# Kernel tuning notes

Hardware: AMD Instinct MI355X
Metric: run time of the kernel (lower is better)

The kernel has to match this reference:

```python
import jax, jax.numpy as jnp
import numpy as np

N_ITER = 4  # n_iter
NEG = -1e9  # masked-score fill (softmax-safe stand-in for -inf)


def _mfvi(x, mask, ternary, global_):
    """MFVI message passing between head (H) and node (Z) variables with global nodes.

    x:       [B, L, D] unary scores for Z nodes
    mask:    [B, L]    padding mask (nonzero = valid token)
    ternary: [D, D, H] ternary factor scores f(Z_i=a, Z_j=b, H-channel c)
    global_: [G, D, H] global-node factor scores
    Defaults: norm=softmax, regularize=1, stepsize=1, damping=0, async_update,
    no tensor decomposition, mode='all-attn', block_msg=False, output_prob=False.
    """
    B, L, D = x.shape
    m1 = (mask != 0)                                             # [B, L]
    pair_valid = m1[:, None, :, None] & m1[:, None, None, :]     # [B, 1, L, L]
    unary = x                                                    # pos_embed='none'
    Qz = jax.nn.softmax(unary, axis=-1)                          # [B, L, D]
    F_Z = unary
    neg = jnp.asarray(NEG, x.dtype)
    for _ in range(N_ITER):
        # --- H update: scores for head variable H_{i,c} over candidate heads j ---
        # F_Hs[n,h,i,j] = sum_{a,b} Qz[n,i,a] * ternary[a,b,h] * Qz[n,j,b]
        F_Hs = jnp.einsum('nia,abh,njb->nhij', Qz, ternary, Qz)  # [B, H, L, L]
        F_Hs = jnp.where(pair_valid, F_Hs, neg)
        # global-node columns: F_Hg[n,h,i,g] = sum_a Qz[n,i,a] * global_[g,a,h]
        F_Hg = jnp.einsum('nia,gah->nhig', Qz, global_)          # [B, H, L, G]
        F_H = jnp.concatenate([F_Hs, F_Hg], axis=-1)             # [B, H, L, L+G]
        Q_H = jax.nn.softmax(F_H, axis=-1)                       # regularize_H = 1
        Qhs, Qhg = Q_H[..., :L], Q_H[..., L:]
        # --- Z update (async: uses fresh Q_H) ---
        # message to Z_i from its chosen head j
        msg_i = jnp.einsum('nhij,njb,abh->nia', Qhs, Qz, ternary)
        # message to Z_j from dependents i (block_msg=False keeps it)
        msg_j = jnp.einsum('nhij,nia,abh->njb', Qhs, Qz, ternary)
        # message to Z_i from global nodes
        msg_g = jnp.einsum('nhig,gah->nia', Qhg, global_)
        F_Z = unary + msg_i + msg_j + msg_g                      # [B, L, D]
        Qz = jax.nn.softmax(F_Z, axis=-1)                        # regularize_Z = 1
    # output_prob=False -> unnormalized scores, zeroed at padding
    return jnp.where(m1[..., None], F_Z, jnp.zeros_like(F_Z))


def setup_inputs() -> dict:
    key = jax.random.key(0)
    k1, k2, k3 = jax.random.split(key, 3)
    B, L, D, H, G = 4, 1024, 128, 8, 64
    x = jax.random.normal(k1, (B, L, D), dtype=jnp.float32)
    mask = jnp.ones((B, L), dtype=jnp.int32)
    ternary = jax.random.normal(k2, (D, D, H), dtype=jnp.float32)          # init std=1
    global_ = jax.random.normal(k3, (G, D, H), dtype=jnp.float32) / np.sqrt(D)
    return {"x": x, "mask": mask, "ternary": ternary, "global_": global_}


def reference(x, mask, ternary, global_):
    return _mfvi(x, mask, ternary, global_)
```

## Files before the change

### kernel.cpp

```cpp
#include <hip/hip_runtime.h>
#include <math.h>

#define Bn 4
#define Ln 1024
#define Dn 128
#define Hn 8
#define Gn 64
#define NITERS 4

typedef _Float16 f16;
typedef _Float16 half8 __attribute__((ext_vector_type(8)));
typedef _Float16 half4v __attribute__((ext_vector_type(4)));
typedef float floatx4 __attribute__((ext_vector_type(4)));

#define WPAD 136
#define PPAD 72

#define MFMA(a, b, c) __builtin_amdgcn_mfma_f32_16x16x32_f16((a), (b), (c), 0, 0, 0)

__device__ __forceinline__ void gl_lds16(const f16* g, f16* l) {
    __builtin_amdgcn_global_load_lds(
        (const __attribute__((address_space(1))) void*)(g),
        (__attribute__((address_space(3))) void*)(l),
        16, 0, 0);
}

__device__ __forceinline__ void issue_tiles(const f16* us, const f16* ub, int sb,
                                            f16* UsB, f16* UbB, int w, int l) {
    #pragma unroll
    for (int k = 0; k < 4; k++) {
        int c = w * 4 + k;
        {
            int r = c * 4 + (l >> 4); int g = (l & 15) ^ (r & 7);
            gl_lds16(us + (size_t)r * Dn + g * 8, UsB + c * 512);
        }
        {
            int r = c * 8 + (l >> 3); int g = (l & 7) ^ (r & 7);
            gl_lds16(ub + (size_t)r * sb + g * 8, UbB + c * 512);
        }
    }
}

__global__ void repack_kernel(const float* __restrict__ ter, const float* __restrict__ glb,
                              f16* __restrict__ TpA, f16* __restrict__ TpB,
                              f16* __restrict__ GpA, f16* __restrict__ Gpt) {
    int idx = blockIdx.x * 256 + threadIdx.x;
    if (idx < Dn * Dn * Hn) {
        int h = idx % Hn; int b = (idx / Hn) % Dn; int a = idx / (Hn * Dn);
        f16 v = (f16)ter[idx];
        TpA[((size_t)h * Dn + a) * Dn + b] = v;
        TpB[((size_t)h * Dn + b) * Dn + a] = v;
    }
    if (idx < Gn * Dn * Hn) {
        int h = idx % Hn; int a = (idx / Hn) % Dn; int g = idx / (Hn * Dn);
        f16 v = (f16)glb[idx];
        GpA[((size_t)h * Gn + g) * Dn + a] = v;
        Gpt[((size_t)h * Dn + a) * Gn + g] = v;
    }
}

__global__ void softmax_rows_kernel(const float* __restrict__ in, f16* __restrict__ out) {
    int row = blockIdx.x;
    int t = threadIdx.x;
    __shared__ float red[2];
    float v = in[(size_t)row * Dn + t];
    float m = v;
    #pragma unroll
    for (int off = 1; off < 64; off <<= 1) m = fmaxf(m, __shfl_xor(m, off, 64));
    if ((t & 63) == 0) red[t >> 6] = m;
    __syncthreads();
    m = fmaxf(red[0], red[1]);
    float e = __expf(v - m);
    float s = e;
    #pragma unroll
    for (int off = 1; off < 64; off <<= 1) s += __shfl_xor(s, off, 64);
    __syncthreads();
    if ((t & 63) == 0) red[t >> 6] = s;
    __syncthreads();
    s = red[0] + red[1];
    out[(size_t)row * Dn + t] = (f16)(e / s);
}

__launch_bounds__(256, 4)
__global__ void uv_kernel(const f16* __restrict__ Qz, const f16* __restrict__ TpA,
                          const f16* __restrict__ TpB,
                          f16* __restrict__ U, f16* __restrict__ Ut, f16* __restrict__ Vt) {
    int bx = blockIdx.x;
    int h  = blockIdx.y;
    int n  = blockIdx.z;
    int t  = threadIdx.x;
    int w = t >> 6, l = t & 63, m = l & 15, q = l >> 4;

    __shared__ __align__(16) f16 Ts[128 * WPAD];

    const f16* qbase = Qz + ((size_t)n * Ln + bx * 64 + w * 16 + m) * Dn;
    half8 aq[4];
    #pragma unroll
    for (int ks = 0; ks < 4; ks++)
        aq[ks] = *(const half8*)(qbase + ks * 32 + q * 8);

    size_t hoff = (size_t)(n * Hn + h);
    int jr0 = bx * 64 + w * 16 + 4 * q;

    {
        const f16* src = TpA + (size_t)h * Dn * Dn;
        for (int ii = 0; ii < 8; ii++) {
            int idx = t + 256 * ii; int r = idx >> 4, c = idx & 15;
            *(float4*)&Ts[r * WPAD + c * 8] = *(const float4*)(src + (size_t)r * Dn + c * 8);
        }
        __syncthreads();
    }
    #pragma unroll
    for (int ct = 0; ct < 8; ct++) {
        floatx4 acc = {0.f, 0.f, 0.f, 0.f};
        #pragma unroll
        for (int ks = 0; ks < 4; ks++) {
            half8 b = *(const half8*)&Ts[(ct * 16 + m) * WPAD + ks * 32 + q * 8];
            acc = MFMA(aq[ks], b, acc);
        }
        half4v pk = { (f16)acc[0], (f16)acc[1], (f16)acc[2], (f16)acc[3] };
        *(half4v*)(Ut + (hoff * Dn + ct * 16 + m) * Ln + jr0) = pk;
    }
    f16* urow = U + (hoff * Ln + (size_t)(bx * 64 + w * 16 + m)) * Dn;
    #pragma unroll
    for (int at = 0; at < 8; at++) {
        floatx4 acc = {0.f, 0.f, 0.f, 0.f};
        #pragma unroll
        for (int ks = 0; ks < 4; ks++) {
            half8 aT = *(const half8*)&Ts[(at * 16 + m) * WPAD + ks * 32 + q * 8];
            acc = MFMA(aT, aq[ks], acc);
        }
        half4v pk = { (f16)acc[0], (f16)acc[1], (f16)acc[2], (f16)acc[3] };
        *(half4v*)(urow + at * 16 + 4 * q) = pk;
    }
    __syncthreads();
    {
        const f16* src = TpB + (size_t)h * Dn * Dn;
        for (int ii = 0; ii < 8; ii++) {
            int idx = t + 256 * ii; int r = idx >> 4, c = idx & 15;
            *(float4*)&Ts[r * WPAD + c * 8] = *(const float4*)(src + (size_t)r * Dn + c * 8);
        }
        __syncthreads();
    }
    #pragma unroll
    for (int ct = 0; ct < 8; ct++) {
        floatx4 acc = {0.f, 0.f, 0.f, 0.f};
        #pragma unroll
        for (int ks = 0; ks < 4; ks++) {
            half8 b = *(const half8*)&Ts[(ct * 16 + m) * WPAD + ks * 32 + q * 8];
            acc = MFMA(aq[ks], b, acc);
        }
        half4v pk = { (f16)acc[0], (f16)acc[1], (f16)acc[2], (f16)acc[3] };
        *(half4v*)(Vt + (hoff * Dn + ct * 16 + m) * Ln + jr0) = pk;
    }
}

__launch_bounds__(256, 2)
__global__ void msgi_kernel(const f16* __restrict__ Qz, const f16* __restrict__ U,
                            const f16* __restrict__ Ut, const f16* __restrict__ GpA,
                            const f16* __restrict__ Gpt, const int* __restrict__ mask,
                            f16* __restrict__ Macc, float* __restrict__ rowLinv) {
    int it = blockIdx.x, h = blockIdx.y, n = blockIdx.z;
    int t = threadIdx.x;
    int w = t >> 6, l = t & 63, m = l & 15, q = l >> 4;
    int rh = w >> 1, ch = w & 1;
    int ih = w >> 1, ah = w & 1;

    __shared__ __align__(16) f16 Us[2][64 * 128];
    __shared__ __align__(16) f16 Ub[2][128 * 64];
    __shared__ __align__(16) f16 Ps[64 * PPAD];
    __shared__ int jms[2][64];
    __shared__ float lpart[2][64];
    __shared__ float linvS[64];

    half8 bq[2][4];
    #pragma unroll
    for (int ib = 0; ib < 2; ib++) {
        const f16* qr = Qz + ((size_t)n * Ln + it * 64 + ch * 32 + ib * 16 + m) * Dn;
        #pragma unroll
        for (int ks = 0; ks < 4; ks++)
            bq[ib][ks] = *(const half8*)(qr + ks * 32 + q * 8);
    }
    int im[2];
    #pragma unroll
    for (int ib = 0; ib < 2; ib++)
        im[ib] = mask[n * Ln + it * 64 + ch * 32 + ib * 16 + m];

    float lacc[2] = {0.f, 0.f};
    floatx4 Oacc[2][4];
    #pragma unroll
    for (int ib = 0; ib < 2; ib++)
        #pragma unroll
        for (int at = 0; at < 4; at++) Oacc[ib][at] = (floatx4){0.f, 0.f, 0.f, 0.f};

    size_t hoff = (size_t)(n * Hn + h);

    issue_tiles(U + hoff * Ln * Dn, Ut + hoff * Dn * Ln, Ln, Us[0], Ub[0], w, l);
    if (t < 64) jms[0][t] = mask[n * Ln + t];
    __syncthreads();

    for (int jt = 0; jt < 17; jt++) {
        int cur = jt & 1, nxt = cur ^ 1;
        if (jt + 1 < 17) {
            const f16 *us, *ub; int sb;
            if (jt + 1 < 16) {
                us = U + (hoff * Ln + (size_t)(jt + 1) * 64) * Dn;
                ub = Ut + hoff * Dn * Ln + (jt + 1) * 64;
                sb = Ln;
            } else {
                us = GpA + (size_t)h * Gn * Dn;
                ub = Gpt + (size_t)h * Dn * Gn;
                sb = Gn;
            }
            issue_tiles(us, ub, sb, Us[nxt], Ub[nxt], w, l);
            if (t < 64) jms[nxt][t] = (jt + 1 < 16) ? mask[n * Ln + (jt + 1) * 64 + t] : 1;
        }
        int isg = (jt == 16);
        #pragma unroll
        for (int jb = 0; jb < 2; jb++) {
            int r0 = rh * 32 + jb * 16 + m;
            half8 au[4];
            #pragma unroll
            for (int ks = 0; ks < 4; ks++)
                au[ks] = *(const half8*)&Us[cur][((size_t)r0 << 7) + ((((ks << 2) + q)) ^ (r0 & 7)) * 8];
            int jmr[4];
            #pragma unroll
            for (int reg = 0; reg < 4; reg++)
                jmr[reg] = jms[cur][rh * 32 + jb * 16 + 4 * q + reg];
            #pragma unroll
            for (int ib = 0; ib < 2; ib++) {
                floatx4 s = {0.f, 0.f, 0.f, 0.f};
                #pragma unroll
                for (int ks = 0; ks < 4; ks++) s = MFMA(au[ks], bq[ib][ks], s);
                half4v pk;
                #pragma unroll
                for (int reg = 0; reg < 4; reg++) {
                    float p = (isg || (im[ib] && jmr[reg])) ? __expf(fminf(s[reg], 11.f)) : 0.f;
                    lacc[ib] += p;
                    pk[reg] = (f16)p;
                }
                *(half4v*)&Ps[(ch * 32 + ib * 16 + m) * PPAD + rh * 32 + jb * 16 + 4 * q] = pk;
            }
        }
        __syncthreads();

        #pragma unroll
        for (int kst = 0; kst < 2; kst++) {
            half8 aP[2];
            #pragma unroll
            for (int ib = 0; ib < 2; ib++)
                aP[ib] = *(const half8*)&Ps[(ih * 32 + ib * 16 + m) * PPAD + kst * 32 + q * 8];
            #pragma unroll
            for (int at = 0; at < 4; at++) {
                int r0 = ah * 64 + at * 16 + m;
                half8 bU = *(const half8*)&Ub[cur][((size_t)r0 << 6) + ((((kst << 2) + q)) ^ (r0 & 7)) * 8];
                #pragma unroll
                for (int ib = 0; ib < 2; ib++)
                    Oacc[ib][at] = MFMA(aP[ib], bU, Oacc[ib][at]);
            }
        }
        __syncthreads();
    }

    #pragma unroll
    for (int ib = 0; ib < 2; ib++) {
        float v = lacc[ib];
        v += __shfl_xor(v, 16, 64);
        v += __shfl_xor(v, 32, 64);
        lacc[ib] = v;
    }
    if (q == 0) {
        lpart[rh][ch * 32 + m] = lacc[0];
        lpart[rh][ch * 32 + 16 + m] = lacc[1];
    }
    __syncthreads();
    size_t rbase = hoff * Ln + (size_t)it * 64;
    if (t < 64) {
        float inv = 1.0f / (lpart[0][t] + lpart[1][t]);
        linvS[t] = inv;
        int mk = mask[n * Ln + it * 64 + t];
        rowLinv[rbase + t] = mk ? inv : 0.f;
    }
    __syncthreads();
    f16* Mo = Macc + rbase * Dn;
    #pragma unroll
    for (int ib = 0; ib < 2; ib++)
        #pragma unroll
        for (int reg = 0; reg < 4; reg++) {
            int row = ih * 32 + ib * 16 + 4 * q + reg;
            float inv = linvS[row];
            #pragma unroll
            for (int at = 0; at < 4; at++)
                Mo[(size_t)row * Dn + ah * 64 + at * 16 + m] = (f16)(Oacc[ib][at][reg] * inv);
        }
}

__launch_bounds__(256, 2)
__global__ void msgj_kernel(const f16* __restrict__ Qz, const f16* __restrict__ U,
                            const f16* __restrict__ Vt, const int* __restrict__ mask,
                            const float* __restrict__ rowLinv, f16* __restrict__ Macc) {
    int jt = blockIdx.x, h = blockIdx.y, n = blockIdx.z;
    int t = threadIdx.x;
    int w = t >> 6, l = t & 63, m = l & 15, q = l >> 4;
    int ihs = w >> 1, jhs = w & 1;
    int jh2 = w >> 1, bh = w & 1;

    __shared__ __align__(16) f16 Qs[2][64 * 128];
    __shared__ __align__(16) f16 Vb[2][128 * 64];
    __shared__ __align__(16) f16 Psj[64 * PPAD];
    __shared__ float lvS[2][64];

    size_t hoff = (size_t)(n * Hn + h);

    half8 bu[2][4];
    #pragma unroll
    for (int jb = 0; jb < 2; jb++) {
        const f16* ur = U + (hoff * Ln + (size_t)jt * 64 + jhs * 32 + jb * 16 + m) * Dn;
        #pragma unroll
        for (int ks = 0; ks < 4; ks++)
            bu[jb][ks] = *(const half8*)(ur + ks * 32 + q * 8);
    }
    int jm[2];
    #pragma unroll
    for (int jb = 0; jb < 2; jb++)
        jm[jb] = mask[n * Ln + jt * 64 + jhs * 32 + jb * 16 + m];

    floatx4 Oacc[2][4];
    #pragma unroll
    for (int jb = 0; jb < 2; jb++)
        #pragma unroll
        for (int bt = 0; bt < 4; bt++) Oacc[jb][bt] = (floatx4){0.f, 0.f, 0.f, 0.f};

    issue_tiles(Qz + (size_t)n * Ln * Dn, Vt + hoff * Dn * Ln, Ln, Qs[0], Vb[0], w, l);
    if (t < 64) lvS[0][t] = rowLinv[hoff * Ln + t];
    __syncthreads();

    for (int it2 = 0; it2 < 16; it2++) {
        int cur = it2 & 1, nxt = cur ^ 1;
        if (it2 + 1 < 16) {
            issue_tiles(Qz + ((size_t)n * Ln + (size_t)(it2 + 1) * 64) * Dn,
                        Vt + hoff * Dn * Ln + (it2 + 1) * 64, Ln, Qs[nxt], Vb[nxt], w, l);
            if (t < 64) lvS[nxt][t] = rowLinv[hoff * Ln + (it2 + 1) * 64 + t];
        }
        #pragma unroll
        for (int ib = 0; ib < 2; ib++) {
            int r0 = ihs * 32 + ib * 16 + m;
            half8 aq2[4];
            #pragma unroll
            for (int ks = 0; ks < 4; ks++)
                aq2[ks] = *(const half8*)&Qs[cur][((size_t)r0 << 7) + ((((ks << 2) + q)) ^ (r0 & 7)) * 8];
            float lv[4];
            #pragma unroll
            for (int reg = 0; reg < 4; reg++)
                lv[reg] = lvS[cur][ihs * 32 + ib * 16 + 4 * q + reg];
            #pragma unroll
            for (int jb = 0; jb < 2; jb++) {
                floatx4 s = {0.f, 0.f, 0.f, 0.f};
                #pragma unroll
                for (int ks = 0; ks < 4; ks++) s = MFMA(aq2[ks], bu[jb][ks], s);
                half4v pk;
                #pragma unroll
                for (int reg = 0; reg < 4; reg++) {
                    float p = jm[jb] ? __expf(fminf(s[reg], 11.f)) * lv[reg] : 0.f;
                    pk[reg] = (f16)p;
                }
                *(half4v*)&Psj[(jhs * 32 + jb * 16 + m) * PPAD + ihs * 32 + ib * 16 + 4 * q] = pk;
            }
        }
        __syncthreads();

        #pragma unroll
        for (int kst = 0; kst < 2; kst++) {
            half8 aP[2];
            #pragma unroll
            for (int jb = 0; jb < 2; jb++)
                aP[jb] = *(const half8*)&Psj[(jh2 * 32 + jb * 16 + m) * PPAD + kst * 32 + q * 8];
            #pragma unroll
            for (int bt = 0; bt < 4; bt++) {
                int r0 = bh * 64 + bt * 16 + m;
                half8 bV = *(const half8*)&Vb[cur][((size_t)r0 << 6) + ((((kst << 2) + q)) ^ (r0 & 7)) * 8];
                #pragma unroll
                for (int jb = 0; jb < 2; jb++)
                    Oacc[jb][bt] = MFMA(aP[jb], bV, Oacc[jb][bt]);
            }
        }
        __syncthreads();
    }

    f16* Mo = Macc + (hoff * Ln + (size_t)jt * 64) * Dn;
    #pragma unroll
    for (int jb = 0; jb < 2; jb++)
        #pragma unroll
        for (int reg = 0; reg < 4; reg++) {
            int row = jh2 * 32 + jb * 16 + 4 * q + reg;
            #pragma unroll
            for (int bt = 0; bt < 4; bt++) {
                f16* p = &Mo[(size_t)row * Dn + bh * 64 + bt * 16 + m];
                *p = (f16)((float)*p + Oacc[jb][bt][reg]);
            }
        }
}

__global__ void combine_kernel(const float* __restrict__ x, const f16* __restrict__ Macc,
                               const int* __restrict__ mask, float* __restrict__ out,
                               f16* __restrict__ Qzh, int do_softmax, int do_mask) {
    int t = threadIdx.x;
    int half = t >> 7;
    int t2 = t & 127;
    int row = blockIdx.x * 2 + half;
    __shared__ float red[4];
    int n = row >> 10;
    float acc = x[(size_t)row * Dn + t2];
    const f16* mp = Macc + (size_t)n * Hn * Ln * Dn + (size_t)(row & 1023) * Dn + t2;
    #pragma unroll
    for (int h = 0; h < Hn; h++) acc += (float)mp[(size_t)h * Ln * Dn];
    float o = acc;
    if (do_mask && mask[row] == 0) o = 0.f;
    out[(size_t)row * Dn + t2] = o;
    if (do_softmax) {
        float m = acc;
        #pragma unroll
        for (int off = 1; off < 64; off <<= 1) m = fmaxf(m, __shfl_xor(m, off, 64));
        if ((t & 63) == 0) red[t >> 6] = m;
        __syncthreads();
        m = fmaxf(red[2 * half], red[2 * half + 1]);
        float e = __expf(acc - m);
        float s = e;
        #pragma unroll
        for (int off = 1; off < 64; off <<= 1) s += __shfl_xor(s, off, 64);
        __syncthreads();
        if ((t & 63) == 0) red[t >> 6] = s;
        __syncthreads();
        s = red[2 * half] + red[2 * half + 1];
        Qzh[(size_t)row * Dn + t2] = (f16)(e / s);
    }
}

extern "C" void kernel_launch(void* const* d_in, const int* in_sizes, int n_in,
                              void* d_out, int out_size, void* d_ws, size_t ws_size,
                              hipStream_t stream) {
    const float* x       = (const float*)d_in[0];
    const int*   mask    = (const int*)d_in[1];
    const float* ternary = (const float*)d_in[2];
    const float* global_ = (const float*)d_in[3];
    float* out = (float*)d_out;
    (void)ws_size; (void)n_in; (void)in_sizes; (void)out_size;

    char* ws = (char*)d_ws;
    size_t o = 0;
    f16* Qzh = (f16*)(ws + o); o += (size_t)Bn * Ln * Dn * 2;
    f16* U   = (f16*)(ws + o); o += (size_t)Bn * Hn * Ln * Dn * 2;
    f16* Ut  = (f16*)(ws + o); o += (size_t)Bn * Hn * Ln * Dn * 2;
    f16* Vt  = (f16*)(ws + o); o += (size_t)Bn * Hn * Ln * Dn * 2;
    f16* TpA = (f16*)(ws + o); o += (size_t)Hn * Dn * Dn * 2;
    f16* TpB = (f16*)(ws + o); o += (size_t)Hn * Dn * Dn * 2;
    f16* GpA = (f16*)(ws + o); o += (size_t)Hn * Gn * Dn * 2;
    f16* Gpt = (f16*)(ws + o); o += (size_t)Hn * Dn * Gn * 2;
    float* rowLinv = (float*)(ws + o); o += (size_t)Bn * Hn * Ln * 4;
    f16* Macc = (f16*)(ws + o); o += (size_t)Bn * Hn * Ln * Dn * 2;

    repack_kernel<<<(Dn * Dn * Hn + 255) / 256, 256, 0, stream>>>(ternary, global_, TpA, TpB, GpA, Gpt);
    softmax_rows_kernel<<<Bn * Ln, 128, 0, stream>>>(x, Qzh);

    for (int it = 0; it < NITERS; it++) {
        uv_kernel<<<dim3(Ln / 64, Hn, Bn), 256, 0, stream>>>(Qzh, TpA, TpB, U, Ut, Vt);
        msgi_kernel<<<dim3(Ln / 64, Hn, Bn), 256, 0, stream>>>(Qzh, U, Ut, GpA, Gpt, mask, Macc, rowLinv);
        msgj_kernel<<<dim3(Ln / 64, Hn, Bn), 256, 0, stream>>>(Qzh, U, Vt, mask, rowLinv, Macc);
        combine_kernel<<<Bn * Ln / 2, 256, 0, stream>>>(x, Macc, mask, out, Qzh,
                                                        (it < NITERS - 1) ? 1 : 0,
                                                        (it == NITERS - 1) ? 1 : 0);
    }
}
```

Measured before the change: 400.6 us.

## Give each warp a private Ub/Vb slice and drop the trailing per-tile barrier

In msgi and msgj, the second GEMM's output is now split by D columns per warp, so each warp reads only its own 32-row slice of the Ub/Vb tile. The warp can then reload that slice itself right after use, so the Ub/Vb buffer drops from double to single buffering. The P buffer becomes double-buffered instead, which lets the second __syncthreads per tile iteration be removed. In exchange, each warp re-reads all 64 P rows, and each warp's private reload is exposed because it is not prefetched a full iteration ahead.

After: 400.7 us. Within noise of the previous version (+0.0%).

```diff
diff --git a/kernel.cpp b/kernel.cpp
--- a/kernel.cpp
+++ b/kernel.cpp
@@ -25,19 +25,21 @@
         16, 0, 0);
 }
 
-__device__ __forceinline__ void issue_tiles(const f16* us, const f16* ub, int sb,
-                                            f16* UsB, f16* UbB, int w, int l) {
+__device__ __forceinline__ void issue_us(const f16* us, f16* UsB, int w, int l) {
     #pragma unroll
     for (int k = 0; k < 4; k++) {
         int c = w * 4 + k;
-        {
-            int r = c * 4 + (l >> 4); int g = (l & 15) ^ (r & 7);
-            gl_lds16(us + (size_t)r * Dn + g * 8, UsB + c * 512);
-        }
-        {
-            int r = c * 8 + (l >> 3); int g = (l & 7) ^ (r & 7);
-            gl_lds16(ub + (size_t)r * sb + g * 8, UbB + c * 512);
-        }
+        int r = c * 4 + (l >> 4); int g = (l & 15) ^ (r & 7);
+        gl_lds16(us + (size_t)r * Dn + g * 8, UsB + c * 512);
+    }
+}
+
+__device__ __forceinline__ void issue_ub_priv(const f16* ub, int sb, f16* UbB, int w, int l) {
+    #pragma unroll
+    for (int k = 0; k < 4; k++) {
+        int r = w * 32 + k * 8 + (l >> 3);
+        int g = (l & 7) ^ (r & 7);
+        gl_lds16(ub + (size_t)r * sb + g * 8, UbB + (w * 32 + k * 8) * 64);
     }
 }
 
@@ -164,11 +166,10 @@
     int t = threadIdx.x;
     int w = t >> 6, l = t & 63, m = l & 15, q = l >> 4;
     int rh = w >> 1, ch = w & 1;
-    int ih = w >> 1, ah = w & 1;
 
     __shared__ __align__(16) f16 Us[2][64 * 128];
-    __shared__ __align__(16) f16 Ub[2][128 * 64];
-    __shared__ __align__(16) f16 Ps[64 * PPAD];
+    __shared__ __align__(16) f16 Ub[128 * 64];
+    __shared__ __align__(16) f16 Ps[2][64 * PPAD];
     __shared__ int jms[2][64];
     __shared__ float lpart[2][64];
     __shared__ float linvS[64];
@@ -187,32 +188,26 @@
         im[ib] = mask[n * Ln + it * 64 + ch * 32 + ib * 16 + m];
 
     float lacc[2] = {0.f, 0.f};
-    floatx4 Oacc[2][4];
-    #pragma unroll
-    for (int ib = 0; ib < 2; ib++)
-        #pragma unroll
-        for (int at = 0; at < 4; at++) Oacc[ib][at] = (floatx4){0.f, 0.f, 0.f, 0.f};
+    floatx4 Oacc[4][2];
+    #pragma unroll
+    for (int ib = 0; ib < 4; ib++) {
+        Oacc[ib][0] = (floatx4){0.f, 0.f, 0.f, 0.f};
+        Oacc[ib][1] = (floatx4){0.f, 0.f, 0.f, 0.f};
+    }
 
     size_t hoff = (size_t)(n * Hn + h);
 
-    issue_tiles(U + hoff * Ln * Dn, Ut + hoff * Dn * Ln, Ln, Us[0], Ub[0], w, l);
+    issue_us(U + hoff * Ln * Dn, Us[0], w, l);
+    issue_ub_priv(Ut + hoff * Dn * Ln, Ln, Ub, w, l);
     if (t < 64) jms[0][t] = mask[n * Ln + t];
     __syncthreads();
 
     for (int jt = 0; jt < 17; jt++) {
-        int cur = jt & 1, nxt = cur ^ 1;
+        int cur = jt & 1, nxt = cur ^ 1, pb = jt & 1;
         if (jt + 1 < 17) {
-            const f16 *us, *ub; int sb;
-            if (jt + 1 < 16) {
-                us = U + (hoff * Ln + (size_t)(jt + 1) * 64) * Dn;
-                ub = Ut + hoff * Dn * Ln + (jt + 1) * 64;
-                sb = Ln;
-            } else {
-                us = GpA + (size_t)h * Gn * Dn;
-                ub = Gpt + (size_t)h * Dn * Gn;
-                sb = Gn;
-            }
-            issue_tiles(us, ub, sb, Us[nxt], Ub[nxt], w, l);
+            const f16* us = (jt + 1 < 16) ? U + (hoff * Ln + (size_t)(jt + 1) * 64) * Dn
+                                          : GpA + (size_t)h * Gn * Dn;
+            issue_us(us, Us[nxt], w, l);
             if (t < 64) jms[nxt][t] = (jt + 1 < 16) ? mask[n * Ln + (jt + 1) * 64 + t] : 1;
         }
         int isg = (jt == 16);
@@ -239,27 +234,33 @@
                     lacc[ib] += p;
                     pk[reg] = (f16)p;
                 }
-                *(half4v*)&Ps[(ch * 32 + ib * 16 + m) * PPAD + rh * 32 + jb * 16 + 4 * q] = pk;
+                *(half4v*)&Ps[pb][(ch * 32 + ib * 16 + m) * PPAD + rh * 32 + jb * 16 + 4 * q] = pk;
             }
         }
         __syncthreads();
 
         #pragma unroll
         for (int kst = 0; kst < 2; kst++) {
-            half8 aP[2];
-            #pragma unroll
-            for (int ib = 0; ib < 2; ib++)
-                aP[ib] = *(const half8*)&Ps[(ih * 32 + ib * 16 + m) * PPAD + kst * 32 + q * 8];
-            #pragma unroll
-            for (int at = 0; at < 4; at++) {
-                int r0 = ah * 64 + at * 16 + m;
-                half8 bU = *(const half8*)&Ub[cur][((size_t)r0 << 6) + ((((kst << 2) + q)) ^ (r0 & 7)) * 8];
-                #pragma unroll
-                for (int ib = 0; ib < 2; ib++)
-                    Oacc[ib][at] = MFMA(aP[ib], bU, Oacc[ib][at]);
+            half8 aP[4];
+            #pragma unroll
+            for (int ib = 0; ib < 4; ib++)
+                aP[ib] = *(const half8*)&Ps[pb][(ib * 16 + m) * PPAD + kst * 32 + q * 8];
+            #pragma unroll
+            for (int bt = 0; bt < 2; bt++) {
+                int r0 = w * 32 + bt * 16 + m;
+                half8 bU = *(const half8*)&Ub[((size_t)r0 << 6) + ((((kst << 2) + q)) ^ (r0 & 7)) * 8];
+                #pragma unroll
+                for (int ib = 0; ib < 4; ib++)
+                    Oacc[ib][bt] = MFMA(aP[ib], bU, Oacc[ib][bt]);
             }
         }
-        __syncthreads();
+        if (jt + 1 < 17) {
+            __builtin_amdgcn_sched_barrier(0);
+            const f16* ub; int sb;
+            if (jt + 1 < 16) { ub = Ut + hoff * Dn * Ln + (jt + 1) * 64; sb = Ln; }
+            else             { ub = Gpt + (size_t)h * Dn * Gn;           sb = Gn; }
+            issue_ub_priv(ub, sb, Ub, w, l);
+        }
     }
 
     #pragma unroll
@@ -284,14 +285,14 @@
     __syncthreads();
     f16* Mo = Macc + rbase * Dn;
     #pragma unroll
-    for (int ib = 0; ib < 2; ib++)
+    for (int ib = 0; ib < 4; ib++)
         #pragma unroll
         for (int reg = 0; reg < 4; reg++) {
-            int row = ih * 32 + ib * 16 + 4 * q + reg;
+            int row = ib * 16 + 4 * q + reg;
             float inv = linvS[row];
             #pragma unroll
-            for (int at = 0; at < 4; at++)
-                Mo[(size_t)row * Dn + ah * 64 + at * 16 + m] = (f16)(Oacc[ib][at][reg] * inv);
+            for (int bt = 0; bt < 2; bt++)
+                Mo[(size_t)row * Dn + w * 32 + bt * 16 + m] = (f16)(Oacc[ib][bt][reg] * inv);
         }
 }
 
@@ -303,11 +304,10 @@
     int t = threadIdx.x;
     int w = t >> 6, l = t & 63, m = l & 15, q = l >> 4;
     int ihs = w >> 1, jhs = w & 1;
-    int jh2 = w >> 1, bh = w & 1;
 
     __shared__ __align__(16) f16 Qs[2][64 * 128];
-    __shared__ __align__(16) f16 Vb[2][128 * 64];
-    __shared__ __align__(16) f16 Psj[64 * PPAD];
+    __shared__ __align__(16) f16 Vb[128 * 64];
+    __shared__ __align__(16) f16 Psj[2][64 * PPAD];
     __shared__ float lvS[2][64];
 
     size_t hoff = (size_t)(n * Hn + h);
@@ -325,21 +325,22 @@
     for (int jb = 0; jb < 2; jb++)
         jm[jb] = mask[n * Ln + jt * 64 + jhs * 32 + jb * 16 + m];
 
-    floatx4 Oacc[2][4];
-    #pragma unroll
-    for (int jb = 0; jb < 2; jb++)
-        #pragma unroll
-        for (int bt = 0; bt < 4; bt++) Oacc[jb][bt] = (floatx4){0.f, 0.f, 0.f, 0.f};
-
-    issue_tiles(Qz + (size_t)n * Ln * Dn, Vt + hoff * Dn * Ln, Ln, Qs[0], Vb[0], w, l);
+    floatx4 Oacc[4][2];
+    #pragma unroll
+    for (int jb = 0; jb < 4; jb++) {
+        Oacc[jb][0] = (floatx4){0.f, 0.f, 0.f, 0.f};
+        Oacc[jb][1] = (floatx4){0.f, 0.f, 0.f, 0.f};
+    }
+
+    issue_us(Qz + (size_t)n * Ln * Dn, Qs[0], w, l);
+    issue_ub_priv(Vt + hoff * Dn * Ln, Ln, Vb, w, l);
     if (t < 64) lvS[0][t] = rowLinv[hoff * Ln + t];
     __syncthreads();
 
     for (int it2 = 0; it2 < 16; it2++) {
-        int cur = it2 & 1, nxt = cur ^ 1;
+        int cur = it2 & 1, nxt = cur ^ 1, pb = it2 & 1;
         if (it2 + 1 < 16) {
-            issue_tiles(Qz + ((size_t)n * Ln + (size_t)(it2 + 1) * 64) * Dn,
-                        Vt + hoff * Dn * Ln + (it2 + 1) * 64, Ln, Qs[nxt], Vb[nxt], w, l);
+            issue_us(Qz + ((size_t)n * Ln + (size_t)(it2 + 1) * 64) * Dn, Qs[nxt], w, l);
             if (t < 64) lvS[nxt][t] = rowLinv[hoff * Ln + (it2 + 1) * 64 + t];
         }
         #pragma unroll
@@ -364,38 +365,41 @@
                     float p = jm[jb] ? __expf(fminf(s[reg], 11.f)) * lv[reg] : 0.f;
                     pk[reg] = (f16)p;
                 }
-                *(half4v*)&Psj[(jhs * 32 + jb * 16 + m) * PPAD + ihs * 32 + ib * 16 + 4 * q] = pk;
+                *(half4v*)&Psj[pb][(jhs * 32 + jb * 16 + m) * PPAD + ihs * 32 + ib * 16 + 4 * q] = pk;
             }
         }
         __syncthreads();
 
         #pragma unroll
         for (int kst = 0; kst < 2; kst++) {
-            half8 aP[2];
-            #pragma unroll
-            for (int jb = 0; jb < 2; jb++)
-                aP[jb] = *(const half8*)&Psj[(jh2 * 32 + jb * 16 + m) * PPAD + kst * 32 + q * 8];
-            #pragma unroll
-            for (int bt = 0; bt < 4; bt++) {
-                int r0 = bh * 64 + bt * 16 + m;
-                half8 bV = *(const half8*)&Vb[cur][((size_t)r0 << 6) + ((((kst << 2) + q)) ^ (r0 & 7)) * 8];
-                #pragma unroll
-                for (int jb = 0; jb < 2; jb++)
+            half8 aP[4];
+            #pragma unroll
+            for (int jb = 0; jb < 4; jb++)
+                aP[jb] = *(const half8*)&Psj[pb][(jb * 16 + m) * PPAD + kst * 32 + q * 8];
+            #pragma unroll
+            for (int bt = 0; bt < 2; bt++) {
+                int r0 = w * 32 + bt * 16 + m;
+                half8 bV = *(const half8*)&Vb[((size_t)r0 << 6) + ((((kst << 2) + q)) ^ (r0 & 7)) * 8];
+                #pragma unroll
+                for (int jb = 0; jb < 4; jb++)
                     Oacc[jb][bt] = MFMA(aP[jb], bV, Oacc[jb][bt]);
             }
         }
-        __syncthreads();
+        if (it2 + 1 < 16) {
+            __builtin_amdgcn_sched_barrier(0);
+            issue_ub_priv(Vt + hoff * Dn * Ln + (it2 + 1) * 64, Ln, Vb, w, l);
+        }
     }
 
     f16* Mo = Macc + (hoff * Ln + (size_t)jt * 64) * Dn;
     #pragma unroll
-    for (int jb = 0; jb < 2; jb++)
+    for (int jb = 0; jb < 4; jb++)
         #pragma unroll
         for (int reg = 0; reg < 4; reg++) {
-            int row = jh2 * 32 + jb * 16 + 4 * q + reg;
-            #pragma unroll
-            for (int bt = 0; bt < 4; bt++) {
-                f16* p = &Mo[(size_t)row * Dn + bh * 64 + bt * 16 + m];
+            int row = jb * 16 + 4 * q + reg;
+            #pragma unroll
+            for (int bt = 0; bt < 2; bt++) {
+                f16* p = &Mo[(size_t)row * Dn + w * 32 + bt * 16 + m];
                 *p = (f16)((float)*p + Oacc[jb][bt][reg]);
             }
         }
```

## Halve query tile in msgi/msgj, drop double buffering, raise occupancy

Applied to the files above, without the earlier changes.

The msgi and msgj kernels now process 32 query rows per block instead of 64, doubling the grid. They drop LDS double-buffering in favour of single buffers loaded synchronously each step, and swizzle the P tile instead of padding it. Launch bounds go from 2 to 4 blocks per CU. The aim is more occupancy and parallelism from less LDS and fewer registers per block, at the cost of losing copy/compute overlap and reloading every key/value tile twice as many times overall.

Measured after the change: 434.9 us. 1.09x slower.

```diff
diff --git a/kernel.cpp b/kernel.cpp
--- a/kernel.cpp
+++ b/kernel.cpp
@@ -14,7 +14,6 @@
 typedef float floatx4 __attribute__((ext_vector_type(4)));
 
 #define WPAD 136
-#define PPAD 72
 
 #define MFMA(a, b, c) __builtin_amdgcn_mfma_f32_16x16x32_f16((a), (b), (c), 0, 0, 0)
 
@@ -25,19 +24,21 @@
         16, 0, 0);
 }
 
-__device__ __forceinline__ void issue_tiles(const f16* us, const f16* ub, int sb,
-                                            f16* UsB, f16* UbB, int w, int l) {
+__device__ __forceinline__ void issue_us(const f16* us, f16* UsB, int w, int l) {
     #pragma unroll
     for (int k = 0; k < 4; k++) {
         int c = w * 4 + k;
-        {
-            int r = c * 4 + (l >> 4); int g = (l & 15) ^ (r & 7);
-            gl_lds16(us + (size_t)r * Dn + g * 8, UsB + c * 512);
-        }
-        {
-            int r = c * 8 + (l >> 3); int g = (l & 7) ^ (r & 7);
-            gl_lds16(ub + (size_t)r * sb + g * 8, UbB + c * 512);
-        }
+        int r = c * 4 + (l >> 4); int g = (l & 15) ^ (r & 7);
+        gl_lds16(us + (size_t)r * Dn + g * 8, UsB + c * 512);
+    }
+}
+
+__device__ __forceinline__ void issue_ub_full(const f16* ub, int sb, f16* UbB, int w, int l) {
+    #pragma unroll
+    for (int k = 0; k < 4; k++) {
+        int c = w * 4 + k;
+        int r = c * 8 + (l >> 3); int g = (l & 7) ^ (r & 7);
+        gl_lds16(ub + (size_t)r * sb + g * 8, UbB + c * 512);
     }
 }
 
@@ -155,7 +156,7 @@
     }
 }
 
-__launch_bounds__(256, 2)
+__launch_bounds__(256, 4)
 __global__ void msgi_kernel(const f16* __restrict__ Qz, const f16* __restrict__ U,
                             const f16* __restrict__ Ut, const f16* __restrict__ GpA,
                             const f16* __restrict__ Gpt, const int* __restrict__ mask,
@@ -166,239 +167,195 @@
     int rh = w >> 1, ch = w & 1;
     int ih = w >> 1, ah = w & 1;
 
-    __shared__ __align__(16) f16 Us[2][64 * 128];
-    __shared__ __align__(16) f16 Ub[2][128 * 64];
-    __shared__ __align__(16) f16 Ps[64 * PPAD];
-    __shared__ int jms[2][64];
-    __shared__ float lpart[2][64];
-    __shared__ float linvS[64];
-
-    half8 bq[2][4];
-    #pragma unroll
-    for (int ib = 0; ib < 2; ib++) {
-        const f16* qr = Qz + ((size_t)n * Ln + it * 64 + ch * 32 + ib * 16 + m) * Dn;
-        #pragma unroll
-        for (int ks = 0; ks < 4; ks++)
-            bq[ib][ks] = *(const half8*)(qr + ks * 32 + q * 8);
-    }
-    int im[2];
-    #pragma unroll
-    for (int ib = 0; ib < 2; ib++)
-        im[ib] = mask[n * Ln + it * 64 + ch * 32 + ib * 16 + m];
-
-    float lacc[2] = {0.f, 0.f};
-    floatx4 Oacc[2][4];
-    #pragma unroll
-    for (int ib = 0; ib < 2; ib++)
-        #pragma unroll
-        for (int at = 0; at < 4; at++) Oacc[ib][at] = (floatx4){0.f, 0.f, 0.f, 0.f};
+    __shared__ __align__(16) f16 Us[64 * 128];
+    __shared__ __align__(16) f16 Ub[128 * 64];
+    __shared__ __align__(16) f16 Ps[32 * 64];
+    __shared__ int jms[64];
+    __shared__ float lpart[2][32];
+    __shared__ float linvS[32];
+
+    const f16* qr = Qz + ((size_t)n * Ln + it * 32 + ch * 16 + m) * Dn;
+    half8 bq[4];
+    #pragma unroll
+    for (int ks = 0; ks < 4; ks++)
+        bq[ks] = *(const half8*)(qr + ks * 32 + q * 8);
+    int im = mask[n * Ln + it * 32 + ch * 16 + m];
+
+    float lacc = 0.f;
+    floatx4 Oacc[4];
+    #pragma unroll
+    for (int at = 0; at < 4; at++) Oacc[at] = (floatx4){0.f, 0.f, 0.f, 0.f};
 
     size_t hoff = (size_t)(n * Hn + h);
 
-    issue_tiles(U + hoff * Ln * Dn, Ut + hoff * Dn * Ln, Ln, Us[0], Ub[0], w, l);
-    if (t < 64) jms[0][t] = mask[n * Ln + t];
-    __syncthreads();
-
     for (int jt = 0; jt < 17; jt++) {
-        int cur = jt & 1, nxt = cur ^ 1;
-        if (jt + 1 < 17) {
-            const f16 *us, *ub; int sb;
-            if (jt + 1 < 16) {
-                us = U + (hoff * Ln + (size_t)(jt + 1) * 64) * Dn;
-                ub = Ut + hoff * Dn * Ln + (jt + 1) * 64;
-                sb = Ln;
-            } else {
-                us = GpA + (size_t)h * Gn * Dn;
-                ub = Gpt + (size_t)h * Dn * Gn;
-                sb = Gn;
-            }
-            issue_tiles(us, ub, sb, Us[nxt], Ub[nxt], w, l);
-            if (t < 64) jms[nxt][t] = (jt + 1 < 16) ? mask[n * Ln + (jt + 1) * 64 + t] : 1;
-        }
+        __syncthreads();
         int isg = (jt == 16);
+        const f16 *us, *ub; int sb;
+        if (!isg) {
+            us = U + (hoff * Ln + (size_t)jt * 64) * Dn;
+            ub = Ut + hoff * Dn * Ln + jt * 64;
+            sb = Ln;
+        } else {
+            us = GpA + (size_t)h * Gn * Dn;
+            ub = Gpt + (size_t)h * Dn * Gn;
+            sb = Gn;
+        }
+        issue_us(us, Us, w, l);
+        issue_ub_full(ub, sb, Ub, w, l);
+        if (t < 64) jms[t] = isg ? 1 : mask[n * Ln + jt * 64 + t];
+        __syncthreads();
+
         #pragma unroll
         for (int jb = 0; jb < 2; jb++) {
             int r0 = rh * 32 + jb * 16 + m;
             half8 au[4];
             #pragma unroll
             for (int ks = 0; ks < 4; ks++)
-                au[ks] = *(const half8*)&Us[cur][((size_t)r0 << 7) + ((((ks << 2) + q)) ^ (r0 & 7)) * 8];
+                au[ks] = *(const half8*)&Us[(size_t)(r0 << 7) + ((((ks << 2) + q)) ^ (r0 & 7)) * 8];
             int jmr[4];
             #pragma unroll
             for (int reg = 0; reg < 4; reg++)
-                jmr[reg] = jms[cur][rh * 32 + jb * 16 + 4 * q + reg];
-            #pragma unroll
-            for (int ib = 0; ib < 2; ib++) {
-                floatx4 s = {0.f, 0.f, 0.f, 0.f};
-                #pragma unroll
-                for (int ks = 0; ks < 4; ks++) s = MFMA(au[ks], bq[ib][ks], s);
-                half4v pk;
-                #pragma unroll
-                for (int reg = 0; reg < 4; reg++) {
-                    float p = (isg || (im[ib] && jmr[reg])) ? __expf(fminf(s[reg], 11.f)) : 0.f;
-                    lacc[ib] += p;
-                    pk[reg] = (f16)p;
-                }
-                *(half4v*)&Ps[(ch * 32 + ib * 16 + m) * PPAD + rh * 32 + jb * 16 + 4 * q] = pk;
+                jmr[reg] = jms[rh * 32 + jb * 16 + 4 * q + reg];
+            floatx4 s = {0.f, 0.f, 0.f, 0.f};
+            #pragma unroll
+            for (int ks = 0; ks < 4; ks++) s = MFMA(au[ks], bq[ks], s);
+            half4v pk;
+            #pragma unroll
+            for (int reg = 0; reg < 4; reg++) {
+                float p = (isg || (im && jmr[reg])) ? __expf(fminf(s[reg], 11.f)) : 0.f;
+                lacc += p;
+                pk[reg] = (f16)p;
             }
+            int i0 = ch * 16 + m;
+            int j4 = rh * 32 + jb * 16 + 4 * q;
+            *(half4v*)&Ps[i0 * 64 + (((j4 >> 3) ^ (i0 & 7)) * 8) + (j4 & 7)] = pk;
         }
         __syncthreads();
 
         #pragma unroll
         for (int kst = 0; kst < 2; kst++) {
-            half8 aP[2];
-            #pragma unroll
-            for (int ib = 0; ib < 2; ib++)
-                aP[ib] = *(const half8*)&Ps[(ih * 32 + ib * 16 + m) * PPAD + kst * 32 + q * 8];
+            int p0 = ih * 16 + m;
+            half8 aP = *(const half8*)&Ps[p0 * 64 + ((((kst << 2) + q)) ^ (p0 & 7)) * 8];
             #pragma unroll
             for (int at = 0; at < 4; at++) {
-                int r0 = ah * 64 + at * 16 + m;
-                half8 bU = *(const half8*)&Ub[cur][((size_t)r0 << 6) + ((((kst << 2) + q)) ^ (r0 & 7)) * 8];
-                #pragma unroll
-                for (int ib = 0; ib < 2; ib++)
-                    Oacc[ib][at] = MFMA(aP[ib], bU, Oacc[ib][at]);
+                int a0 = ah * 64 + at * 16 + m;
+                half8 bU = *(const half8*)&Ub[(size_t)(a0 << 6) + ((((kst << 2) + q)) ^ (a0 & 7)) * 8];
+                Oacc[at] = MFMA(aP, bU, Oacc[at]);
             }
         }
-        __syncthreads();
-    }
-
-    #pragma unroll
-    for (int ib = 0; ib < 2; ib++) {
-        float v = lacc[ib];
+    }
+
+    {
+        float v = lacc;
         v += __shfl_xor(v, 16, 64);
         v += __shfl_xor(v, 32, 64);
-        lacc[ib] = v;
-    }
-    if (q == 0) {
-        lpart[rh][ch * 32 + m] = lacc[0];
-        lpart[rh][ch * 32 + 16 + m] = lacc[1];
-    }
-    __syncthreads();
-    size_t rbase = hoff * Ln + (size_t)it * 64;
-    if (t < 64) {
+        if (q == 0) lpart[rh][ch * 16 + m] = v;
+    }
+    __syncthreads();
+    size_t rbase = hoff * Ln + (size_t)it * 32;
+    if (t < 32) {
         float inv = 1.0f / (lpart[0][t] + lpart[1][t]);
         linvS[t] = inv;
-        int mk = mask[n * Ln + it * 64 + t];
+        int mk = mask[n * Ln + it * 32 + t];
         rowLinv[rbase + t] = mk ? inv : 0.f;
     }
     __syncthreads();
     f16* Mo = Macc + rbase * Dn;
     #pragma unroll
-    for (int ib = 0; ib < 2; ib++)
-        #pragma unroll
-        for (int reg = 0; reg < 4; reg++) {
-            int row = ih * 32 + ib * 16 + 4 * q + reg;
-            float inv = linvS[row];
-            #pragma unroll
-            for (int at = 0; at < 4; at++)
-                Mo[(size_t)row * Dn + ah * 64 + at * 16 + m] = (f16)(Oacc[ib][at][reg] * inv);
-        }
-}
-
-__launch_bounds__(256, 2)
+    for (int reg = 0; reg < 4; reg++) {
+        int row = ih * 16 + 4 * q + reg;
+        float inv = linvS[row];
+        #pragma unroll
+        for (int at = 0; at < 4; at++)
+            Mo[(size_t)row * Dn + ah * 64 + at * 16 + m] = (f16)(Oacc[at][reg] * inv);
+    }
+}
+
+__launch_bounds__(256, 4)
 __global__ void msgj_kernel(const f16* __restrict__ Qz, const f16* __restrict__ U,
                             const f16* __restrict__ Vt, const int* __restrict__ mask,
                             const float* __restrict__ rowLinv, f16* __restrict__ Macc) {
     int jt = blockIdx.x, h = blockIdx.y, n = blockIdx.z;
     int t = threadIdx.x;
     int w = t >> 6, l = t & 63, m = l & 15, q = l >> 4;
-    int ihs = w >> 1, jhs = w & 1;
-    int jh2 = w >> 1, bh = w & 1;
-
-    __shared__ __align__(16) f16 Qs[2][64 * 128];
-    __shared__ __align__(16) f16 Vb[2][128 * 64];
-    __shared__ __align__(16) f16 Psj[64 * PPAD];
-    __shared__ float lvS[2][64];
+    int rh = w >> 1, ch = w & 1;
+    int jh = w >> 1, bh = w & 1;
+
+    __shared__ __align__(16) f16 Qs[64 * 128];
+    __shared__ __align__(16) f16 Vb[128 * 64];
+    __shared__ __align__(16) f16 Psj[32 * 64];
+    __shared__ float lvS[64];
 
     size_t hoff = (size_t)(n * Hn + h);
 
-    half8 bu[2][4];
-    #pragma unroll
-    for (int jb = 0; jb < 2; jb++) {
-        const f16* ur = U + (hoff * Ln + (size_t)jt * 64 + jhs * 32 + jb * 16 + m) * Dn;
-        #pragma unroll
-        for (int ks = 0; ks < 4; ks++)
-            bu[jb][ks] = *(const half8*)(ur + ks * 32 + q * 8);
-    }
-    int jm[2];
-    #pragma unroll
-    for (int jb = 0; jb < 2; jb++)
-        jm[jb] = mask[n * Ln + jt * 64 + jhs * 32 + jb * 16 + m];
-
-    floatx4 Oacc[2][4];
-    #pragma unroll
-    for (int jb = 0; jb < 2; jb++)
-        #pragma unroll
-        for (int bt = 0; bt < 4; bt++) Oacc[jb][bt] = (floatx4){0.f, 0.f, 0.f, 0.f};
-
-    issue_tiles(Qz + (size_t)n * Ln * Dn, Vt + hoff * Dn * Ln, Ln, Qs[0], Vb[0], w, l);
-    if (t < 64) lvS[0][t] = rowLinv[hoff * Ln + t];
-    __syncthreads();
+    const f16* ur = U + (hoff * Ln + (size_t)jt * 32 + ch * 16 + m) * Dn;
+    half8 bu[4];
+    #pragma unroll
+    for (int ks = 0; ks < 4; ks++)
+        bu[ks] = *(const half8*)(ur + ks * 32 + q * 8);
+    int jm = mask[n * Ln + jt * 32 + ch * 16 + m];
+
+    floatx4 Oacc[4];
+    #pragma unroll
+    for (int bt = 0; bt < 4; bt++) Oacc[bt] = (floatx4){0.f, 0.f, 0.f, 0.f};
 
     for (int it2 = 0; it2 < 16; it2++) {
-        int cur = it2 & 1, nxt = cur ^ 1;
-        if (it2 + 1 < 16) {
-            issue_tiles(Qz + ((size_t)n * Ln + (size_t)(it2 + 1) * 64) * Dn,
-                        Vt + hoff * Dn * Ln + (it2 + 1) * 64, Ln, Qs[nxt], Vb[nxt], w, l);
-            if (t < 64) lvS[nxt][t] = rowLinv[hoff * Ln + (it2 + 1) * 64 + t];
-        }
+        __syncthreads();
+        issue_us(Qz + ((size_t)n * Ln + (size_t)it2 * 64) * Dn, Qs, w, l);
+        issue_ub_full(Vt + hoff * Dn * Ln + it2 * 64, Ln, Vb, w, l);
+        if (t < 64) lvS[t] = rowLinv[hoff * Ln + it2 * 64 + t];
+        __syncthreads();
+
         #pragma unroll
         for (int ib = 0; ib < 2; ib++) {
-            int r0 = ihs * 32 + ib * 16 + m;
+            int r0 = rh * 32 + ib * 16 + m;
             half8 aq2[4];
             #pragma unroll
             for (int ks = 0; ks < 4; ks++)
-                aq2[ks] = *(const half8*)&Qs[cur][((size_t)r0 << 7) + ((((ks << 2) + q)) ^ (r0 & 7)) * 8];
+                aq2[ks] = *(const half8*)&Qs[(size_t)(r0 << 7) + ((((ks << 2) + q)) ^ (r0 & 7)) * 8];
             float lv[4];
             #pragma unroll
             for (int reg = 0; reg < 4; reg++)
-                lv[reg] = lvS[cur][ihs * 32 + ib * 16 + 4 * q + reg];
-            #pragma unroll
-            for (int jb = 0; jb < 2; jb++) {
-                floatx4 s = {0.f, 0.f, 0.f, 0.f};
-                #pragma unroll
-                for (int ks = 0; ks < 4; ks++) s = MFMA(aq2[ks], bu[jb][ks], s);
-                half4v pk;
-                #pragma unroll
-                for (int reg = 0; reg < 4; reg++) {
-                    float p = jm[jb] ? __expf(fminf(s[reg], 11.f)) * lv[reg] : 0.f;
-                    pk[reg] = (f16)p;
-                }
-                *(half4v*)&Psj[(jhs * 32 + jb * 16 + m) * PPAD + ihs * 32 + ib * 16 + 4 * q] = pk;
+                lv[reg] = lvS[rh * 32 + ib * 16 + 4 * q + reg];
+            floatx4 s = {0.f, 0.f, 0.f, 0.f};
+            #pragma unroll
+            for (int ks = 0; ks < 4; ks++) s = MFMA(aq2[ks], bu[ks], s);
+            half4v pk;
+            #pragma unroll
+            for (int reg = 0; reg < 4; reg++) {
+                float p = jm ? __expf(fminf(s[reg], 11.f)) * lv[reg] : 0.f;
+                pk[reg] = (f16)p;
             }
+            int j0 = ch * 16 + m;
+            int i4 = rh * 32 + ib * 16 + 4 * q;
+            *(half4v*)&Psj[j0 * 64 + (((i4 >> 3) ^ (j0 & 7)) * 8) + (i4 & 7)] = pk;
         }
         __syncthreads();
 
         #pragma unroll
         for (int kst = 0; kst < 2; kst++) {
-            half8 aP[2];
-            #pragma unroll
-            for (int jb = 0; jb < 2; jb++)
-                aP[jb] = *(const half8*)&Psj[(jh2 * 32 + jb * 16 + m) * PPAD + kst * 32 + q * 8];
+            int p0 = jh * 16 + m;
+            half8 aP = *(const half8*)&Psj[p0 * 64 + ((((kst << 2) + q)) ^ (p0 & 7)) * 8];
             #pragma unroll
             for (int bt = 0; bt < 4; bt++) {
-                int r0 = bh * 64 + bt * 16 + m;
-                half8 bV = *(const half8*)&Vb[cur][((size_t)r0 << 6) + ((((kst << 2) + q)) ^ (r0 & 7)) * 8];
-                #pragma unroll
-                for (int jb = 0; jb < 2; jb++)
-                    Oacc[jb][bt] = MFMA(aP[jb], bV, Oacc[jb][bt]);
+                int b0 = bh * 64 + bt * 16 + m;
+                half8 bV = *(const half8*)&Vb[(size_t)(b0 << 6) + ((((kst << 2) + q)) ^ (b0 & 7)) * 8];
+                Oacc[bt] = MFMA(aP, bV, Oacc[bt]);
             }
         }
-        __syncthreads();
-    }
-
-    f16* Mo = Macc + (hoff * Ln + (size_t)jt * 64) * Dn;
-    #pragma unroll
-    for (int jb = 0; jb < 2; jb++)
-        #pragma unroll
-        for (int reg = 0; reg < 4; reg++) {
-            int row = jh2 * 32 + jb * 16 + 4 * q + reg;
-            #pragma unroll
-            for (int bt = 0; bt < 4; bt++) {
-                f16* p = &Mo[(size_t)row * Dn + bh * 64 + bt * 16 + m];
-                *p = (f16)((float)*p + Oacc[jb][bt][reg]);
-            }
-        }
+    }
+
+    f16* Mo = Macc + (hoff * Ln + (size_t)jt * 32) * Dn;
+    #pragma unroll
+    for (int reg = 0; reg < 4; reg++) {
+        int row = jh * 16 + 4 * q + reg;
+        #pragma unroll
+        for (int bt = 0; bt < 4; bt++) {
+            f16* p = &Mo[(size_t)row * Dn + bh * 64 + bt * 16 + m];
+            *p = (f16)((float)*p + Oacc[bt][reg]);
+        }
+    }
 }
 
 __global__ void combine_kernel(const float* __restrict__ x, const f16* __restrict__ Macc,
@@ -464,8 +421,8 @@
 
     for (int it = 0; it < NITERS; it++) {
         uv_kernel<<<dim3(Ln / 64, Hn, Bn), 256, 0, stream>>>(Qzh, TpA, TpB, U, Ut, Vt);
-        msgi_kernel<<<dim3(Ln / 64, Hn, Bn), 256, 0, stream>>>(Qzh, U, Ut, GpA, Gpt, mask, Macc, rowLinv);
-        msgj_kernel<<<dim3(Ln / 64, Hn, Bn), 256, 0, stream>>>(Qzh, U, Vt, mask, rowLinv, Macc);
+        msgi_kernel<<<dim3(Ln / 32, Hn, Bn), 256, 0, stream>>>(Qzh, U, Ut, GpA, Gpt, mask, Macc, rowLinv);
+        msgj_kernel<<<dim3(Ln / 32, Hn, Bn), 256, 0, stream>>>(Qzh, U, Vt, mask, rowLinv, Macc);
         combine_kernel<<<Bn * Ln / 2, 256, 0, stream>>>(x, Macc, mask, out, Qzh,
                                                         (it < NITERS - 1) ? 1 : 0,
                                                         (it == NITERS - 1) ? 1 : 0);
```
